# Kernel tuning notes

Measured on AMD Instinct MI355X. Metric: run time of the kernel, lower is better.

## Reference

```python
import jax, jax.numpy as jnp
import numpy as np

N_A = 50000
N_B = 50000
E = 500000
HID = 128
NEG_SLOPE = 0.2
LN_EPS = 1e-5


def _ln(x, g, b):
    mu = jnp.mean(x, axis=-1, keepdims=True)
    var = jnp.mean((x - mu) ** 2, axis=-1, keepdims=True)
    return (x - mu) * jax.lax.rsqrt(var + LN_EPS) * g + b


def _gat(x_src, x_dst, src, dst, W, a_src, a_dst, bias, H, D, n_dst):
    # PyG GATConv (shared lin for src/dst, add_self_loops=False, eval mode)
    hs = (x_src @ W).reshape(-1, H, D)              # [N_src, H, D]
    hd = (x_dst @ W).reshape(-1, H, D)              # [N_dst, H, D]
    a_s = jnp.einsum('nhd,hd->nh', hs, a_src)       # per-node src score
    a_d = jnp.einsum('nhd,hd->nh', hd, a_dst)       # per-node dst score
    e = jax.nn.leaky_relu(a_s[src] + a_d[dst], NEG_SLOPE)   # [E, H]
    m = jax.ops.segment_max(e, dst, num_segments=n_dst)     # segment softmax
    m = jnp.where(jnp.isfinite(m), m, 0.0)
    ex = jnp.exp(e - m[dst])
    s = jax.ops.segment_sum(ex, dst, num_segments=n_dst)
    alpha = ex / (s[dst] + 1e-16)                   # [E, H]
    msg = hs[src] * alpha[:, :, None]               # [E, H, D]
    out = jax.ops.segment_sum(msg, dst, num_segments=n_dst) # [N_dst, H, D]
    return out.reshape(n_dst, H * D) + bias


def setup_inputs() -> dict:
    key = jax.random.key(0)
    ks = jax.random.split(key, 32)
    f32 = jnp.float32

    def rn(k, sh, s=0.05):
        return jax.random.normal(k, sh, dtype=f32) * s

    inp = {}
    inp['x_A'] = jax.random.normal(ks[0], (N_A, 128), dtype=f32)
    inp['x_B'] = jax.random.normal(ks[1], (N_B, 64), dtype=f32)
    inp['pWA'] = rn(ks[2], (128, HID)); inp['pbA'] = rn(ks[3], (HID,))
    inp['pWB'] = rn(ks[4], (64, HID)); inp['pbB'] = rn(ks[5], (HID,))
    inp['w0ab'] = rn(ks[6], (HID, HID)); inp['as0ab'] = rn(ks[7], (4, 32))
    inp['ad0ab'] = rn(ks[8], (4, 32)); inp['b0ab'] = rn(ks[9], (HID,))
    inp['w0ba'] = rn(ks[10], (HID, HID)); inp['as0ba'] = rn(ks[11], (4, 32))
    inp['ad0ba'] = rn(ks[12], (4, 32)); inp['b0ba'] = rn(ks[13], (HID,))
    inp['w1ab'] = rn(ks[14], (HID, HID)); inp['as1ab'] = rn(ks[15], (1, HID))
    inp['ad1ab'] = rn(ks[16], (1, HID)); inp['b1ab'] = rn(ks[17], (HID,))
    inp['w1ba'] = rn(ks[18], (HID, HID)); inp['as1ba'] = rn(ks[19], (1, HID))
    inp['ad1ba'] = rn(ks[20], (1, HID)); inp['b1ba'] = rn(ks[21], (HID,))
    for i, nm in enumerate(['0A', '0B', '1A', '1B']):
        inp['g' + nm] = jnp.ones((HID,), dtype=f32)
        inp['bn' + nm] = jnp.zeros((HID,), dtype=f32)
    inp['ei_AB'] = jax.random.randint(ks[22], (2, E), 0, N_B)  # src in A, dst in B
    inp['ei_BA'] = jax.random.randint(ks[23], (2, E), 0, N_A)  # src in B, dst in A
    return inp


def reference(x_A, x_B, pWA, pbA, pWB, pbB,
              w0ab, as0ab, ad0ab, b0ab, w0ba, as0ba, ad0ba, b0ba,
              w1ab, as1ab, ad1ab, b1ab, w1ba, as1ba, ad1ba, b1ba,
              g0A, bn0A, g0B, bn0B, g1A, bn1A, g1B, bn1B,
              ei_AB, ei_BA):
    # input projections (dropout is eval-mode no-op)
    hA = x_A @ pWA + pbA
    hB = x_B @ pWB + pbB
    # layer 0: heads=4, d_head=32, concat -> 128
    pA, pB = hA, hB
    nB = _gat(hA, hB, ei_AB[0], ei_AB[1], w0ab, as0ab, ad0ab, b0ab, 4, 32, N_B)
    nA = _gat(hB, hA, ei_BA[0], ei_BA[1], w0ba, as0ba, ad0ba, b0ba, 4, 32, N_A)
    hA = jax.nn.relu(_ln(nA, g0A, bn0A)) + pA
    hB = jax.nn.relu(_ln(nB, g0B, bn0B)) + pB
    # layer 1: heads=1, out=128
    pA, pB = hA, hB
    nB = _gat(hA, hB, ei_AB[0], ei_AB[1], w1ab, as1ab, ad1ab, b1ab, 1, HID, N_B)
    nA = _gat(hB, hA, ei_BA[0], ei_BA[1], w1ba, as1ba, ad1ba, b1ba, 1, HID, N_A)
    hA = jax.nn.relu(_ln(nA, g1A, bn1A)) + pA
    hB = jax.nn.relu(_ln(nB, g1B, bn1B)) + pB
    return hA, hB
```

## Files before the change

kernel.cpp:

```cpp
#include <hip/hip_runtime.h>
#include <hip/hip_bf16.h>

using bf16 = __hip_bfloat16;
using frag8 = __attribute__((ext_vector_type(8))) short;
using f32x4 = __attribute__((ext_vector_type(4))) float;

__device__ __forceinline__ short f2bf_bits(float f) {
  bf16 h = __float2bfloat16(f);
  short s; __builtin_memcpy(&s, &h, 2); return s;
}
__device__ __forceinline__ float bfbits2f(unsigned short u) {
  unsigned uu = (unsigned)u << 16; float f; __builtin_memcpy(&f, &uu, 4); return f;
}
__device__ __forceinline__ float wred_sum(float v) {
#pragma unroll
  for (int o = 32; o; o >>= 1) v += __shfl_xor(v, o);
  return v;
}

struct ConvJob { const void* src; void* dst; int n; int mode; int ksh; };
struct ConvJobs { ConvJob j[28]; };
struct WtJob { const void* wraw; const void* adraw; bf16* out; int H; };
struct WtJobs4 { WtJob j[4]; };

__global__ __launch_bounds__(256) void prep_k(
    const unsigned* __restrict__ xdet, int* __restrict__ flag,
    ConvJobs cjobs, int ncv, WtJobs4 wjobs,
    int* __restrict__ cntA, int nA, int* __restrict__ cntB, int nB)
{
  const int b = blockIdx.x, tid = threadIdx.x;
  if (b >= ncv + 4) {
    int i = (b - (ncv + 4)) * 256 + tid;
    if (i < nA) cntA[i] = 0;
    else if (i < nA + nB) cntB[i - nA] = 0;
    return;
  }
  __shared__ int sh[256];
  int c = 0;
  for (int i = tid; i < 4096; i += 256) {
    unsigned bb = (xdet[i] >> 8) & 0x7F;
    c += (bb >= 0x3B && bb <= 0x41) ? 1 : 0;
  }
  sh[tid] = c; __syncthreads();
  for (int off = 128; off; off >>= 1) { if (tid < off) sh[tid] += sh[tid + off]; __syncthreads(); }
  const int f = (sh[0] < 2048) ? 1 : 0;
  if (b == 0 && tid == 0) flag[0] = f;

  if (b < ncv) {
    ConvJob J = cjobs.j[b];
    const int Kt = 1 << J.ksh;
    for (int i = tid; i < J.n; i += 256) {
      int si = i;
      if (J.mode == 1) { int n = i >> J.ksh, k = i & (Kt - 1); si = k * 128 + n; }
      float v = f ? ((const float*)J.src)[si] : bfbits2f(((const unsigned short*)J.src)[si]);
      if (J.mode == 1) ((bf16*)J.dst)[i] = __float2bfloat16(v);
      else             ((float*)J.dst)[i] = v;
    }
  } else {
    WtJob J = wjobs.j[b - ncv];
    const int H = J.H, D = 128 / H;
    for (int idx = tid; idx < 16 * 128; idx += 256) {
      int h = idx >> 7, k = idx & 127;
      float s = 0.f;
      if (h < H) {
        for (int d = 0; d < D; d++) {
          int n = h * D + d;
          float wv = f ? ((const float*)J.wraw)[k * 128 + n]
                       : bfbits2f(((const unsigned short*)J.wraw)[k * 128 + n]);
          float av = f ? ((const float*)J.adraw)[n]
                       : bfbits2f(((const unsigned short*)J.adraw)[n]);
          s += wv * av;
        }
      }
      J.out[idx] = __float2bfloat16(s);
    }
  }
}

__global__ void hist2_k(const int* __restrict__ dAB, const int* __restrict__ dBA, int E,
                        int* __restrict__ cntB, int* __restrict__ cntA, int geh) {
  int b = blockIdx.x;
  if (b < geh) { int i = b * 256 + threadIdx.x; if (i < E) atomicAdd(&cntB[dAB[i]], 1); }
  else { int i = (b - geh) * 256 + threadIdx.x; if (i < E) atomicAdd(&cntA[dBA[i]], 1); }
}
__device__ __forceinline__ void blocksum_body(const int* cnt, int N, int* bsum, int blk) {
  __shared__ int sh[256];
  const int tid = threadIdx.x;
  const int beg = blk * 1024;
  const int end = (beg + 1024 < N) ? beg + 1024 : N;
  int loc = 0;
  for (int i = beg + tid; i < end; i += 256) loc += cnt[i];
  sh[tid] = loc; __syncthreads();
  for (int off = 128; off; off >>= 1) { if (tid < off) sh[tid] += sh[tid + off]; __syncthreads(); }
  if (tid == 0) bsum[blk] = sh[0];
}
__global__ void blocksum2_k(const int* __restrict__ cntB, int NB, int* __restrict__ bsumB, int nbB,
                            const int* __restrict__ cntA, int NA, int* __restrict__ bsumA) {
  int b = blockIdx.x;
  if (b < nbB) blocksum_body(cntB, NB, bsumB, b);
  else         blocksum_body(cntA, NA, bsumA, b - nbB);
}
__device__ __forceinline__ void scanpart_body(int* bsum, int nb) {
  __shared__ int sh[256];
  const int tid = threadIdx.x;
  int v = (tid < nb) ? bsum[tid] : 0;
  sh[tid] = v; __syncthreads();
  for (int off = 1; off < 256; off <<= 1) {
    int x = sh[tid];
    int o = (tid >= off) ? sh[tid - off] : 0;
    __syncthreads();
    sh[tid] = x + o;
    __syncthreads();
  }
  if (tid < nb) bsum[tid] = (tid == 0) ? 0 : sh[tid - 1];
}
__global__ void scanpart2_k(int* __restrict__ bsumB, int nbB, int* __restrict__ bsumA, int nbA) {
  if (blockIdx.x == 0) scanpart_body(bsumB, nbB);
  else                 scanpart_body(bsumA, nbA);
}
__device__ __forceinline__ void writerp_body(const int* cnt, int N, const int* bsum,
                                             int* rp, int* cur, int blk) {
  __shared__ int sh[256];
  const int tid = threadIdx.x;
  const int idx0 = blk * 1024 + tid * 4;
  int c[4]; int loc = 0;
#pragma unroll
  for (int j = 0; j < 4; j++) {
    int i = idx0 + j;
    c[j] = (i < N) ? cnt[i] : 0;
    loc += c[j];
  }
  sh[tid] = loc; __syncthreads();
  for (int off = 1; off < 256; off <<= 1) {
    int x = sh[tid];
    int o = (tid >= off) ? sh[tid - off] : 0;
    __syncthreads();
    sh[tid] = x + o;
    __syncthreads();
  }
  int run = bsum[blk] + ((tid == 0) ? 0 : sh[tid - 1]);
#pragma unroll
  for (int j = 0; j < 4; j++) {
    int i = idx0 + j;
    if (i < N) { rp[i] = run; cur[i] = run; }
    run += c[j];
  }
  if (idx0 <= N - 1 && N - 1 < idx0 + 4) rp[N] = run;
}
__global__ void writerp2_k(const int* __restrict__ cntB, int NB, const int* __restrict__ bsumB,
                           int* __restrict__ rpAB, int* __restrict__ curB, int nbB,
                           const int* __restrict__ cntA, int NA, const int* __restrict__ bsumA,
                           int* __restrict__ rpBA, int* __restrict__ curA) {
  int b = blockIdx.x;
  if (b < nbB) writerp_body(cntB, NB, bsumB, rpAB, curB, b);
  else         writerp_body(cntA, NA, bsumA, rpBA, curA, b - nbB);
}
__global__ void scatter2_k(const int* __restrict__ sAB, const int* __restrict__ dAB,
                           int* __restrict__ curB, int* __restrict__ slAB,
                           const int* __restrict__ sBA, const int* __restrict__ dBA,
                           int* __restrict__ curA, int* __restrict__ slBA, int E, int geh) {
  int b = blockIdx.x;
  if (b < geh) {
    int i = b * 256 + threadIdx.x;
    if (i < E) { int d = dAB[i]; int pos = atomicAdd(&curB[d], 1); slAB[pos] = sAB[i]; }
  } else {
    int i = (b - geh) * 256 + threadIdx.x;
    if (i < E) { int d = dBA[i]; int pos = atomicAdd(&curA[d], 1); slBA[pos] = sBA[i]; }
  }
}

struct GemmJob {
  const void* Av; const bf16* WT; const float* bias; const float* avec;
  bf16* outFull; float* outScore; const int* flagp;
  const bf16* WT2; float* outScore2;
  int M, K, H, H2;
};
__global__ __launch_bounds__(256) void gemm2_k(GemmJob ja, GemmJob jb, int split) {
  const bool first = blockIdx.x < split;
  const GemmJob J = first ? ja : jb;
  const int blk = first ? blockIdx.x : blockIdx.x - split;

  __shared__ __align__(16) bf16 Wt[128 * 136];
  __shared__ __align__(16) bf16 Wt2s[16 * 136];
  const int tid = threadIdx.x;
  const int K = J.K;
  const int isf32 = J.flagp ? J.flagp[0] : 0;
  const int stride = K + 8;
  const int ksh2 = (K == 128) ? 4 : 3;
  const int kunits = K >> 3;
  for (int u = tid; u < 128 * kunits; u += 256) {
    int n = u >> ksh2, kb = u & (kunits - 1);
    frag8 v = *(const frag8*)(J.WT + n * K + kb * 8);
    *(frag8*)(Wt + n * stride + kb * 8) = v;
  }
  if (J.WT2) {
    int n = tid >> 4, kb = tid & 15;
    *(frag8*)(Wt2s + n * 136 + kb * 8) = *(const frag8*)(J.WT2 + n * 128 + kb * 8);
  }
  __syncthreads();

  const int lane = tid & 63, wave = tid >> 6;
  const int quad = lane >> 4, c = lane & 15;
  const int mbase = blk * 64 + wave * 16;
  const int arow = mbase + c;
  const bool rowOK = arow < J.M;

  f32x4 acc[8];
#pragma unroll
  for (int t = 0; t < 8; t++) acc[t] = (f32x4){0.f, 0.f, 0.f, 0.f};
  f32x4 acc2 = (f32x4){0.f, 0.f, 0.f, 0.f};

  for (int ks = 0; ks < K; ks += 32) {
    frag8 af;
    const int k0 = ks + quad * 8;
    if (rowOK) {
      if (isf32) {
        const float4* ap = (const float4*)((const float*)J.Av + (size_t)arow * K + k0);
        float4 v0 = ap[0], v1 = ap[1];
        af[0] = f2bf_bits(v0.x); af[1] = f2bf_bits(v0.y);
        af[2] = f2bf_bits(v0.z); af[3] = f2bf_bits(v0.w);
        af[4] = f2bf_bits(v1.x); af[5] = f2bf_bits(v1.y);
        af[6] = f2bf_bits(v1.z); af[7] = f2bf_bits(v1.w);
      } else {
        af = *(const frag8*)((const bf16*)J.Av + (size_t)arow * K + k0);
      }
    } else {
#pragma unroll
      for (int j = 0; j < 8; j++) af[j] = 0;
    }
#pragma unroll
    for (int t = 0; t < 8; t++) {
      frag8 bfv = *(const frag8*)(Wt + (t * 16 + c) * stride + k0);
      acc[t] = __builtin_amdgcn_mfma_f32_16x16x32_bf16(af, bfv, acc[t], 0, 0, 0);
    }
    if (J.WT2) {
      frag8 b2 = *(const frag8*)(Wt2s + c * 136 + k0);
      acc2 = __builtin_amdgcn_mfma_f32_16x16x32_bf16(af, b2, acc2, 0, 0, 0);
    }
  }

  if (J.outFull) {
#pragma unroll
    for (int t = 0; t < 8; t++) {
#pragma unroll
      for (int r = 0; r < 4; r++) {
        int orow = mbase + quad * 4 + r;
        if (orow < J.M) {
          float v = acc[t][r];
          if (J.bias) v += J.bias[t * 16 + c];
          J.outFull[(size_t)orow * 128 + t * 16 + c] = __float2bfloat16(v);
        }
      }
    }
  }
  if (J.outScore) {
    const int H = J.H;
    const int TPH = 8 / H;
    for (int hh = 0; hh < H; hh++) {
#pragma unroll
      for (int r = 0; r < 4; r++) {
        float p = 0.f;
        for (int tt = 0; tt < TPH; tt++) {
          int t = hh * TPH + tt;
          p += acc[t][r] * J.avec[t * 16 + c];
        }
#pragma unroll
        for (int off = 1; off < 16; off <<= 1) p += __shfl_xor(p, off);
        int orow = mbase + quad * 4 + r;
        if (c == 0 && orow < J.M) J.outScore[(size_t)orow * H + hh] = p;
      }
    }
  }
  if (J.outScore2) {
#pragma unroll
    for (int r = 0; r < 4; r++) {
      int orow = mbase + quad * 4 + r;
      if (c < J.H2 && orow < J.M) J.outScore2[(size_t)orow * J.H2 + c] = acc2[r];
    }
  }
}

struct AggJob {
  const int* rp; const int* srcl; const float* as_; const float* ad_;
  const bf16* hs; const float* bias; const float* gamma; const float* beta;
  const bf16* resid; bf16* outBf; void* outFinal; const int* flagp;
  int nodeBase, N;
};
template<int H, bool FINAL>
__global__ __launch_bounds__(256) void agg2_k(AggJob JA, AggJob JB, int split) {
  const bool first = blockIdx.x < split;
  const AggJob J = first ? JA : JB;
  const int blk = first ? blockIdx.x : blockIdx.x - split;

  __shared__ int   s_src[4][64];
  __shared__ float s_p[4][64 * H];
  const int wave = threadIdx.x >> 6, lane = threadIdx.x & 63;
  const int n = blk * 4 + wave;
  if (n >= J.N) return;

  const int beg = J.rp[n], end = J.rp[n + 1];
  const int myh = (H == 4) ? (lane >> 4) : 0;
  float4 adv;
  if (H == 4) adv = *(const float4*)(J.ad_ + (size_t)n * 4);
  else        adv.x = J.ad_[n];
  float sl_[H];
#pragma unroll
  for (int h = 0; h < H; h++) sl_[h] = 0.f;
  float acc0 = 0.f, acc1 = 0.f;

  for (int base = beg; base < end; base += 64) {
    const int cn = min(64, end - base);
    if (lane < cn) {
      int s = J.srcl[base + lane];
      s_src[wave][lane] = s;
      if (H == 4) {
        float4 a = *(const float4*)(J.as_ + (size_t)s * 4);
        float4 o; float v;
        v = a.x + adv.x; v = v > 0.f ? v : 0.2f * v; o.x = __expf(v);
        v = a.y + adv.y; v = v > 0.f ? v : 0.2f * v; o.y = __expf(v);
        v = a.z + adv.z; v = v > 0.f ? v : 0.2f * v; o.z = __expf(v);
        v = a.w + adv.w; v = v > 0.f ? v : 0.2f * v; o.w = __expf(v);
        *(float4*)&s_p[wave][lane * 4] = o;
        sl_[0] += o.x; sl_[1] += o.y; sl_[2] += o.z; sl_[3] += o.w;
      } else {
        float v = J.as_[s] + adv.x;
        v = v > 0.f ? v : 0.2f * v;
        float pv = __expf(v);
        s_p[wave][lane] = pv;
        sl_[0] += pv;
      }
    }
    __builtin_amdgcn_wave_barrier();
#pragma unroll 2
    for (int e = 0; e < cn; e++) {
      int src = s_src[wave][e];
      float p = s_p[wave][e * H + myh];
      unsigned u = *(const unsigned*)(J.hs + (size_t)src * 128 + 2 * lane);
      acc0 += p * bfbits2f((unsigned short)(u & 0xFFFF));
      acc1 += p * bfbits2f((unsigned short)(u >> 16));
    }
    __builtin_amdgcn_wave_barrier();
  }

  float s = 0.f;
#pragma unroll
  for (int h = 0; h < H; h++) {
    float t = wred_sum(sl_[h]);
    if (h == myh) s = t;
  }
  const float inv = 1.f / (s + 1e-16f);
  float2 bi = *(const float2*)(J.bias + 2 * lane);
  float y0 = acc0 * inv + bi.x;
  float y1 = acc1 * inv + bi.y;

  float tsum = wred_sum(y0 + y1);
  float tsq  = wred_sum(y0 * y0 + y1 * y1);
  float mu = tsum * 0.0078125f;
  float var = tsq * 0.0078125f - mu * mu;
  float rs = rsqrtf(var + 1e-5f);
  float2 ga = *(const float2*)(J.gamma + 2 * lane);
  float2 be = *(const float2*)(J.beta + 2 * lane);
  float z0 = (y0 - mu) * rs * ga.x + be.x;
  float z1 = (y1 - mu) * rs * ga.y + be.y;
  unsigned ru = *(const unsigned*)(J.resid + (size_t)n * 128 + 2 * lane);
  z0 = fmaxf(z0, 0.f) + bfbits2f((unsigned short)(ru & 0xFFFF));
  z1 = fmaxf(z1, 0.f) + bfbits2f((unsigned short)(ru >> 16));

  if constexpr (FINAL) {
    size_t oi = (size_t)(J.nodeBase + n) * 128 + 2 * lane;
    if (J.flagp[0]) {
      *(float2*)((float*)J.outFinal + oi) = make_float2(z0, z1);
    } else {
      unsigned short l0 = (unsigned short)f2bf_bits(z0);
      unsigned short l1 = (unsigned short)f2bf_bits(z1);
      *(unsigned*)((bf16*)J.outFinal + oi) = (unsigned)l0 | ((unsigned)l1 << 16);
    }
  } else {
    unsigned short l0 = (unsigned short)f2bf_bits(z0);
    unsigned short l1 = (unsigned short)f2bf_bits(z1);
    *(unsigned*)(J.outBf + (size_t)n * 128 + 2 * lane) = (unsigned)l0 | ((unsigned)l1 << 16);
  }
}

extern "C" void kernel_launch(void* const* d_in, const int* in_sizes, int n_in,
                              void* d_out, int out_size, void* d_ws, size_t ws_size,
                              hipStream_t stream)
{
  const int NA = in_sizes[0] / 128;
  const int NB = in_sizes[1] / 64;
  const int E  = in_sizes[30] / 2;
  const int* eiAB = (const int*)d_in[30];
  const int* eiBA = (const int*)d_in[31];
  const int* srcAB = eiAB;  const int* dstAB = eiAB + E;
  const int* srcBA = eiBA;  const int* dstBA = eiBA + E;

  char* w = (char*)d_ws;
  size_t used = 0;
  auto alloc = [&](size_t bytes) {
    char* p = w + used;
    used += (bytes + 255) & ~size_t(255);
    return (void*)p;
  };
  int*  flag  = (int*)alloc(256);
  bf16* WcA   = (bf16*)alloc(16384 * 2);
  bf16* WcB   = (bf16*)alloc(8192 * 2);
  bf16* Wc0ab = (bf16*)alloc(16384 * 2);
  bf16* Wc0ba = (bf16*)alloc(16384 * 2);
  bf16* Wc1ab = (bf16*)alloc(16384 * 2);
  bf16* Wc1ba = (bf16*)alloc(16384 * 2);
  bf16* Wt0ab = (bf16*)alloc(16 * 128 * 2);
  bf16* Wt0ba = (bf16*)alloc(16 * 128 * 2);
  bf16* Wt1ab = (bf16*)alloc(16 * 128 * 2);
  bf16* Wt1ba = (bf16*)alloc(16 * 128 * 2);
  float* vec  = (float*)alloc(22 * 128 * 4);
  bf16* hA    = (bf16*)alloc((size_t)NA * 128 * 2);
  bf16* hB    = (bf16*)alloc((size_t)NB * 128 * 2);
  bf16* hsAB  = (bf16*)alloc((size_t)NA * 128 * 2);
  bf16* hsBA  = (bf16*)alloc((size_t)NB * 128 * 2);
  float* asAB = (float*)alloc((size_t)NA * 4 * 4);
  float* adAB = (float*)alloc((size_t)NB * 4 * 4);
  float* asBA = (float*)alloc((size_t)NB * 4 * 4);
  float* adBA = (float*)alloc((size_t)NA * 4 * 4);
  int* rpAB = (int*)alloc((size_t)(NB + 1) * 4);
  int* slAB = (int*)alloc((size_t)E * 4);
  int* rpBA = (int*)alloc((size_t)(NA + 1) * 4);
  int* slBA = (int*)alloc((size_t)E * 4);
  int* cntA = (int*)alloc((size_t)NA * 4);
  int* curA = (int*)alloc((size_t)NA * 4);
  int* cntB = (int*)alloc((size_t)NB * 4);
  int* curB = (int*)alloc((size_t)NB * 4);
  int* bsumA = (int*)alloc(256 * 4);
  int* bsumB = (int*)alloc(256 * 4);
  if (used > ws_size) return;

  auto V = [&](int i) { return vec + 128 * i; };

  ConvJobs jobs{};
  int nj = 0;
  auto addT = [&](const void* s, void* d, int K) {
    int ksh = (K == 128) ? 7 : 6;
    jobs.j[nj++] = ConvJob{s, d, 128 * K, 1, ksh};
  };
  auto addV = [&](const void* s, void* d) { jobs.j[nj++] = ConvJob{s, d, 128, 0, 7}; };
  addT(d_in[2], WcA, 128);
  addT(d_in[4], WcB, 64);
  addT(d_in[6], Wc0ab, 128);
  addT(d_in[10], Wc0ba, 128);
  addT(d_in[14], Wc1ab, 128);
  addT(d_in[18], Wc1ba, 128);
  const int vsrc[22] = {3, 5, 7, 8, 9, 11, 12, 13, 15, 16, 17, 19, 20, 21, 22, 23, 24, 25, 26, 27, 28, 29};
  for (int i = 0; i < 22; i++) addV(d_in[vsrc[i]], V(i));

  WtJobs4 wj{};
  wj.j[0] = WtJob{d_in[6],  d_in[8],  Wt0ab, 4};
  wj.j[1] = WtJob{d_in[10], d_in[12], Wt0ba, 4};
  wj.j[2] = WtJob{d_in[14], d_in[16], Wt1ab, 1};
  wj.j[3] = WtJob{d_in[18], d_in[20], Wt1ba, 1};

  const int nz = (NA + NB + 255) / 256;
  prep_k<<<nj + 4 + nz, 256, 0, stream>>>((const unsigned*)d_in[0], flag, jobs, nj, wj,
                                          cntA, NA, cntB, NB);

  const int nbB = (NB + 1023) / 1024, nbA = (NA + 1023) / 1024;
  const int geh = (E + 255) / 256;
  hist2_k<<<2 * geh, 256, 0, stream>>>(dstAB, dstBA, E, cntB, cntA, geh);
  blocksum2_k<<<nbB + nbA, 256, 0, stream>>>(cntB, NB, bsumB, nbB, cntA, NA, bsumA);
  scanpart2_k<<<2, 256, 0, stream>>>(bsumB, nbB, bsumA, nbA);
  writerp2_k<<<nbB + nbA, 256, 0, stream>>>(cntB, NB, bsumB, rpAB, curB, nbB,
                                            cntA, NA, bsumA, rpBA, curA);
  scatter2_k<<<2 * geh, 256, 0, stream>>>(srcAB, dstAB, curB, slAB,
                                          srcBA, dstBA, curA, slBA, E, geh);

  const int gA = (NA + 63) / 64, gB = (NB + 63) / 64;
  const int aA = (NA + 3) / 4, aB = (NB + 3) / 4;

  {
    GemmJob ja{d_in[0], WcA, V(0), nullptr, hA, nullptr, flag, nullptr, nullptr, NA, 128, 1, 0};
    GemmJob jb{d_in[1], WcB, V(1), nullptr, hB, nullptr, flag, nullptr, nullptr, NB, 64, 1, 0};
    gemm2_k<<<gA + gB, 256, 0, stream>>>(ja, jb, gA);
  }
  {
    GemmJob ja{hA, Wc0ab, nullptr, V(2), hsAB, asAB, nullptr, Wt0ba, adBA, NA, 128, 4, 4};
    GemmJob jb{hB, Wc0ba, nullptr, V(5), hsBA, asBA, nullptr, Wt0ab, adAB, NB, 128, 4, 4};
    gemm2_k<<<gA + gB, 256, 0, stream>>>(ja, jb, gA);
  }
  {
    AggJob ja{rpAB, slAB, asAB, adAB, hsAB, V(4), V(16), V(17), hB, hB, nullptr, nullptr, 0, NB};
    AggJob jb{rpBA, slBA, asBA, adBA, hsBA, V(7), V(14), V(15), hA, hA, nullptr, nullptr, 0, NA};
    agg2_k<4, false><<<aB + aA, 256, 0, stream>>>(ja, jb, aB);
  }
  {
    GemmJob ja{hA, Wc1ab, nullptr, V(8),  hsAB, asAB, nullptr, Wt1ba, adBA, NA, 128, 1, 1};
    GemmJob jb{hB, Wc1ba, nullptr, V(11), hsBA, asBA, nullptr, Wt1ab, adAB, NB, 128, 1, 1};
    gemm2_k<<<gA + gB, 256, 0, stream>>>(ja, jb, gA);
  }
  {
    AggJob ja{rpAB, slAB, asAB, adAB, hsAB, V(10), V(20), V(21), hB, nullptr, d_out, flag, NA, NB};
    AggJob jb{rpBA, slBA, asBA, adBA, hsBA, V(13), V(18), V(19), hA, nullptr, d_out, flag, 0, NA};
    agg2_k<1, true><<<aB + aA, 256, 0, stream>>>(ja, jb, aB);
  }
}
```

Measured before the change: 480.5 us.

## Fuse CSR build into GEMM launches, partition scatter, split aggregation by head count

The edge histogram now runs as extra blocks inside the input-projection GEMM launch. The prefix scan is collapsed into two single-block scans that run alongside the layer-0 GEMM. This removes four separate launches and the multi-level scan. The scatter is rewritten so each block handles only one eighth of the destination range, which is meant to improve atomic and write locality. Aggregation is split into specialised 4-head and 1-head kernels that use readfirstlane scalar loads; the 1-head path drops shared-memory staging and computes the softmax inline per edge. The single-block scan is serial per thread over about 200 entries each and may become a long tail inside the GEMM launch.

```diff
diff --git a/kernel.cpp b/kernel.cpp
--- a/kernel.cpp
+++ b/kernel.cpp
@@ -16,6 +16,11 @@
 #pragma unroll
   for (int o = 32; o; o >>= 1) v += __shfl_xor(v, o);
   return v;
+}
+__device__ __forceinline__ float rfl_f(float v) {
+  int i; __builtin_memcpy(&i, &v, 4);
+  i = __builtin_amdgcn_readfirstlane(i);
+  float f; __builtin_memcpy(&f, &i, 4); return f;
 }
 
 struct ConvJob { const void* src; void* dst; int n; int mode; int ksh; };
@@ -77,109 +82,13 @@
   }
 }
 
-__global__ void hist2_k(const int* __restrict__ dAB, const int* __restrict__ dBA, int E,
-                        int* __restrict__ cntB, int* __restrict__ cntA, int geh) {
-  int b = blockIdx.x;
-  if (b < geh) { int i = b * 256 + threadIdx.x; if (i < E) atomicAdd(&cntB[dAB[i]], 1); }
-  else { int i = (b - geh) * 256 + threadIdx.x; if (i < E) atomicAdd(&cntA[dBA[i]], 1); }
-}
-__device__ __forceinline__ void blocksum_body(const int* cnt, int N, int* bsum, int blk) {
-  __shared__ int sh[256];
-  const int tid = threadIdx.x;
-  const int beg = blk * 1024;
-  const int end = (beg + 1024 < N) ? beg + 1024 : N;
-  int loc = 0;
-  for (int i = beg + tid; i < end; i += 256) loc += cnt[i];
-  sh[tid] = loc; __syncthreads();
-  for (int off = 128; off; off >>= 1) { if (tid < off) sh[tid] += sh[tid + off]; __syncthreads(); }
-  if (tid == 0) bsum[blk] = sh[0];
-}
-__global__ void blocksum2_k(const int* __restrict__ cntB, int NB, int* __restrict__ bsumB, int nbB,
-                            const int* __restrict__ cntA, int NA, int* __restrict__ bsumA) {
-  int b = blockIdx.x;
-  if (b < nbB) blocksum_body(cntB, NB, bsumB, b);
-  else         blocksum_body(cntA, NA, bsumA, b - nbB);
-}
-__device__ __forceinline__ void scanpart_body(int* bsum, int nb) {
-  __shared__ int sh[256];
-  const int tid = threadIdx.x;
-  int v = (tid < nb) ? bsum[tid] : 0;
-  sh[tid] = v; __syncthreads();
-  for (int off = 1; off < 256; off <<= 1) {
-    int x = sh[tid];
-    int o = (tid >= off) ? sh[tid - off] : 0;
-    __syncthreads();
-    sh[tid] = x + o;
-    __syncthreads();
-  }
-  if (tid < nb) bsum[tid] = (tid == 0) ? 0 : sh[tid - 1];
-}
-__global__ void scanpart2_k(int* __restrict__ bsumB, int nbB, int* __restrict__ bsumA, int nbA) {
-  if (blockIdx.x == 0) scanpart_body(bsumB, nbB);
-  else                 scanpart_body(bsumA, nbA);
-}
-__device__ __forceinline__ void writerp_body(const int* cnt, int N, const int* bsum,
-                                             int* rp, int* cur, int blk) {
-  __shared__ int sh[256];
-  const int tid = threadIdx.x;
-  const int idx0 = blk * 1024 + tid * 4;
-  int c[4]; int loc = 0;
-#pragma unroll
-  for (int j = 0; j < 4; j++) {
-    int i = idx0 + j;
-    c[j] = (i < N) ? cnt[i] : 0;
-    loc += c[j];
-  }
-  sh[tid] = loc; __syncthreads();
-  for (int off = 1; off < 256; off <<= 1) {
-    int x = sh[tid];
-    int o = (tid >= off) ? sh[tid - off] : 0;
-    __syncthreads();
-    sh[tid] = x + o;
-    __syncthreads();
-  }
-  int run = bsum[blk] + ((tid == 0) ? 0 : sh[tid - 1]);
-#pragma unroll
-  for (int j = 0; j < 4; j++) {
-    int i = idx0 + j;
-    if (i < N) { rp[i] = run; cur[i] = run; }
-    run += c[j];
-  }
-  if (idx0 <= N - 1 && N - 1 < idx0 + 4) rp[N] = run;
-}
-__global__ void writerp2_k(const int* __restrict__ cntB, int NB, const int* __restrict__ bsumB,
-                           int* __restrict__ rpAB, int* __restrict__ curB, int nbB,
-                           const int* __restrict__ cntA, int NA, const int* __restrict__ bsumA,
-                           int* __restrict__ rpBA, int* __restrict__ curA) {
-  int b = blockIdx.x;
-  if (b < nbB) writerp_body(cntB, NB, bsumB, rpAB, curB, b);
-  else         writerp_body(cntA, NA, bsumA, rpBA, curA, b - nbB);
-}
-__global__ void scatter2_k(const int* __restrict__ sAB, const int* __restrict__ dAB,
-                           int* __restrict__ curB, int* __restrict__ slAB,
-                           const int* __restrict__ sBA, const int* __restrict__ dBA,
-                           int* __restrict__ curA, int* __restrict__ slBA, int E, int geh) {
-  int b = blockIdx.x;
-  if (b < geh) {
-    int i = b * 256 + threadIdx.x;
-    if (i < E) { int d = dAB[i]; int pos = atomicAdd(&curB[d], 1); slAB[pos] = sAB[i]; }
-  } else {
-    int i = (b - geh) * 256 + threadIdx.x;
-    if (i < E) { int d = dBA[i]; int pos = atomicAdd(&curA[d], 1); slBA[pos] = sBA[i]; }
-  }
-}
-
 struct GemmJob {
   const void* Av; const bf16* WT; const float* bias; const float* avec;
   bf16* outFull; float* outScore; const int* flagp;
   const bf16* WT2; float* outScore2;
   int M, K, H, H2;
 };
-__global__ __launch_bounds__(256) void gemm2_k(GemmJob ja, GemmJob jb, int split) {
-  const bool first = blockIdx.x < split;
-  const GemmJob J = first ? ja : jb;
-  const int blk = first ? blockIdx.x : blockIdx.x - split;
-
+__device__ __forceinline__ void gemm_body(const GemmJob& J, int blk) {
   __shared__ __align__(16) bf16 Wt[128 * 136];
   __shared__ __align__(16) bf16 Wt2s[16 * 136];
   const int tid = threadIdx.x;
@@ -280,79 +189,105 @@
   }
 }
 
+__global__ __launch_bounds__(256) void histgemm_k(
+    GemmJob ja, GemmJob jb, int gsplit,
+    const int* __restrict__ dAB, const int* __restrict__ dBA, int E, int geh,
+    int* __restrict__ cntB, int* __restrict__ cntA)
+{
+  const int b = blockIdx.x;
+  if (b < 2 * geh) {
+    if (b < geh) { int i = b * 256 + threadIdx.x; if (i < E) atomicAdd(&cntB[dAB[i]], 1); }
+    else { int i = (b - geh) * 256 + threadIdx.x; if (i < E) atomicAdd(&cntA[dBA[i]], 1); }
+    return;
+  }
+  const int gb = b - 2 * geh;
+  if (gb < gsplit) gemm_body(ja, gb);
+  else             gemm_body(jb, gb - gsplit);
+}
+
+__device__ __forceinline__ void scanfull_body(const int* __restrict__ cnt, int N,
+                                              int* __restrict__ rp, int* __restrict__ cur) {
+  __shared__ int sh[256];
+  const int tid = threadIdx.x;
+  const int seg = (N + 255) / 256;
+  const int b0 = tid * seg < N ? tid * seg : N;
+  const int b1 = (tid + 1) * seg < N ? (tid + 1) * seg : N;
+  int loc = 0;
+  for (int i = b0; i < b1; i++) loc += cnt[i];
+  sh[tid] = loc; __syncthreads();
+  for (int off = 1; off < 256; off <<= 1) {
+    int x = sh[tid];
+    int o = (tid >= off) ? sh[tid - off] : 0;
+    __syncthreads();
+    sh[tid] = x + o;
+    __syncthreads();
+  }
+  int run = (tid == 0) ? 0 : sh[tid - 1];
+  for (int i = b0; i < b1; i++) { rp[i] = run; cur[i] = run; run += cnt[i]; }
+  if (tid == 255) rp[N] = run;
+}
+__global__ __launch_bounds__(256) void scangemm_k(
+    GemmJob ja, GemmJob jb, int gsplit,
+    const int* __restrict__ cntB, int NB, int* __restrict__ rpAB, int* __restrict__ curB,
+    const int* __restrict__ cntA, int NA, int* __restrict__ rpBA, int* __restrict__ curA)
+{
+  const int b = blockIdx.x;
+  if (b < 2) {
+    if (b == 0) scanfull_body(cntB, NB, rpAB, curB);
+    else        scanfull_body(cntA, NA, rpBA, curA);
+    return;
+  }
+  const int gb = b - 2;
+  if (gb < gsplit) gemm_body(ja, gb);
+  else             gemm_body(jb, gb - gsplit);
+}
+
+__global__ __launch_bounds__(256) void gemm2_k(GemmJob ja, GemmJob jb, int split) {
+  if (blockIdx.x < split) gemm_body(ja, blockIdx.x);
+  else                    gemm_body(jb, blockIdx.x - split);
+}
+
+__global__ __launch_bounds__(256) void scatter8_k(
+    const int* __restrict__ sAB, const int* __restrict__ dAB,
+    const int* __restrict__ sBA, const int* __restrict__ dBA, int E,
+    int* __restrict__ curB, int* __restrict__ slAB,
+    int* __restrict__ curA, int* __restrict__ slBA, int NB, int NA)
+{
+  const int g = blockIdx.x & 7;
+  const int sidx = blockIdx.x >> 3;
+  const int loB = (int)((long long)NB * g >> 3), hiB = (int)((long long)NB * (g + 1) >> 3);
+  const int loA = (int)((long long)NA * g >> 3), hiA = (int)((long long)NA * (g + 1) >> 3);
+  const int b0 = sidx * 2048;
+#pragma unroll
+  for (int j = 0; j < 8; j++) {
+    int i = b0 + j * 256 + threadIdx.x;
+    if (i < 2 * E) {
+      bool ab = i < E;
+      int k = ab ? i : i - E;
+      int d = ab ? dAB[k] : dBA[k];
+      int lo = ab ? loB : loA, hi = ab ? hiB : hiA;
+      if (d >= lo && d < hi) {
+        int sv = ab ? sAB[k] : sBA[k];
+        int pos = atomicAdd((ab ? curB : curA) + d, 1);
+        (ab ? slAB : slBA)[pos] = sv;
+      }
+    }
+  }
+}
+
 struct AggJob {
   const int* rp; const int* srcl; const float* as_; const float* ad_;
   const bf16* hs; const float* bias; const float* gamma; const float* beta;
   const bf16* resid; bf16* outBf; void* outFinal; const int* flagp;
   int nodeBase, N;
 };
-template<int H, bool FINAL>
-__global__ __launch_bounds__(256) void agg2_k(AggJob JA, AggJob JB, int split) {
-  const bool first = blockIdx.x < split;
-  const AggJob J = first ? JA : JB;
-  const int blk = first ? blockIdx.x : blockIdx.x - split;
-
-  __shared__ int   s_src[4][64];
-  __shared__ float s_p[4][64 * H];
-  const int wave = threadIdx.x >> 6, lane = threadIdx.x & 63;
-  const int n = blk * 4 + wave;
-  if (n >= J.N) return;
-
-  const int beg = J.rp[n], end = J.rp[n + 1];
-  const int myh = (H == 4) ? (lane >> 4) : 0;
-  float4 adv;
-  if (H == 4) adv = *(const float4*)(J.ad_ + (size_t)n * 4);
-  else        adv.x = J.ad_[n];
-  float sl_[H];
-#pragma unroll
-  for (int h = 0; h < H; h++) sl_[h] = 0.f;
-  float acc0 = 0.f, acc1 = 0.f;
-
-  for (int base = beg; base < end; base += 64) {
-    const int cn = min(64, end - base);
-    if (lane < cn) {
-      int s = J.srcl[base + lane];
-      s_src[wave][lane] = s;
-      if (H == 4) {
-        float4 a = *(const float4*)(J.as_ + (size_t)s * 4);
-        float4 o; float v;
-        v = a.x + adv.x; v = v > 0.f ? v : 0.2f * v; o.x = __expf(v);
-        v = a.y + adv.y; v = v > 0.f ? v : 0.2f * v; o.y = __expf(v);
-        v = a.z + adv.z; v = v > 0.f ? v : 0.2f * v; o.z = __expf(v);
-        v = a.w + adv.w; v = v > 0.f ? v : 0.2f * v; o.w = __expf(v);
-        *(float4*)&s_p[wave][lane * 4] = o;
-        sl_[0] += o.x; sl_[1] += o.y; sl_[2] += o.z; sl_[3] += o.w;
-      } else {
-        float v = J.as_[s] + adv.x;
-        v = v > 0.f ? v : 0.2f * v;
-        float pv = __expf(v);
-        s_p[wave][lane] = pv;
-        sl_[0] += pv;
-      }
-    }
-    __builtin_amdgcn_wave_barrier();
-#pragma unroll 2
-    for (int e = 0; e < cn; e++) {
-      int src = s_src[wave][e];
-      float p = s_p[wave][e * H + myh];
-      unsigned u = *(const unsigned*)(J.hs + (size_t)src * 128 + 2 * lane);
-      acc0 += p * bfbits2f((unsigned short)(u & 0xFFFF));
-      acc1 += p * bfbits2f((unsigned short)(u >> 16));
-    }
-    __builtin_amdgcn_wave_barrier();
-  }
-
-  float s = 0.f;
-#pragma unroll
-  for (int h = 0; h < H; h++) {
-    float t = wred_sum(sl_[h]);
-    if (h == myh) s = t;
-  }
-  const float inv = 1.f / (s + 1e-16f);
+
+template<bool FINAL>
+__device__ __forceinline__ void agg_epilogue(const AggJob& J, int n, int lane,
+                                             float inv, float acc0, float acc1) {
   float2 bi = *(const float2*)(J.bias + 2 * lane);
   float y0 = acc0 * inv + bi.x;
   float y1 = acc1 * inv + bi.y;
-
   float tsum = wred_sum(y0 + y1);
   float tsq  = wred_sum(y0 * y0 + y1 * y1);
   float mu = tsum * 0.0078125f;
@@ -365,7 +300,6 @@
   unsigned ru = *(const unsigned*)(J.resid + (size_t)n * 128 + 2 * lane);
   z0 = fmaxf(z0, 0.f) + bfbits2f((unsigned short)(ru & 0xFFFF));
   z1 = fmaxf(z1, 0.f) + bfbits2f((unsigned short)(ru >> 16));
-
   if constexpr (FINAL) {
     size_t oi = (size_t)(J.nodeBase + n) * 128 + 2 * lane;
     if (J.flagp[0]) {
@@ -380,6 +314,92 @@
     unsigned short l1 = (unsigned short)f2bf_bits(z1);
     *(unsigned*)(J.outBf + (size_t)n * 128 + 2 * lane) = (unsigned)l0 | ((unsigned)l1 << 16);
   }
+}
+
+template<bool FINAL>
+__global__ __launch_bounds__(256) void agg4_k(AggJob JA, AggJob JB, int split) {
+  const bool first = blockIdx.x < split;
+  const AggJob J = first ? JA : JB;
+  const int blk = first ? blockIdx.x : blockIdx.x - split;
+
+  __shared__ float s_p[4][64 * 4];
+  const int lane = threadIdx.x & 63;
+  const int wave = __builtin_amdgcn_readfirstlane(threadIdx.x >> 6);
+  const int n = blk * 4 + wave;
+  if (n >= J.N) return;
+
+  const int beg = __builtin_amdgcn_readfirstlane(J.rp[n]);
+  const int end = __builtin_amdgcn_readfirstlane(J.rp[n + 1]);
+  const int myh = lane >> 4;
+  const float4 adv = *(const float4*)(J.ad_ + (size_t)n * 4);
+  float sl0 = 0.f, sl1 = 0.f, sl2 = 0.f, sl3 = 0.f;
+  float acc0 = 0.f, acc1 = 0.f;
+  const int* srcp = J.srcl;
+  const bf16* hsp = J.hs;
+
+  for (int base = beg; base < end; base += 64) {
+    const int cn = (end - base < 64) ? end - base : 64;
+    if (lane < cn) {
+      int s = srcp[base + lane];
+      float4 a = *(const float4*)(J.as_ + (size_t)s * 4);
+      float4 o; float v;
+      v = a.x + adv.x; v = v > 0.f ? v : 0.2f * v; o.x = __expf(v);
+      v = a.y + adv.y; v = v > 0.f ? v : 0.2f * v; o.y = __expf(v);
+      v = a.z + adv.z; v = v > 0.f ? v : 0.2f * v; o.z = __expf(v);
+      v = a.w + adv.w; v = v > 0.f ? v : 0.2f * v; o.w = __expf(v);
+      *(float4*)&s_p[wave][lane * 4] = o;
+      sl0 += o.x; sl1 += o.y; sl2 += o.z; sl3 += o.w;
+    }
+    __builtin_amdgcn_wave_barrier();
+#pragma unroll 4
+    for (int e = 0; e < cn; e++) {
+      const int src = __builtin_amdgcn_readfirstlane(srcp[base + e]);
+      const float p = s_p[wave][e * 4 + myh];
+      const unsigned u = *(const unsigned*)(hsp + (size_t)src * 128 + 2 * lane);
+      acc0 += p * bfbits2f((unsigned short)(u & 0xFFFF));
+      acc1 += p * bfbits2f((unsigned short)(u >> 16));
+    }
+    __builtin_amdgcn_wave_barrier();
+  }
+
+  float t0 = wred_sum(sl0), t1 = wred_sum(sl1), t2 = wred_sum(sl2), t3 = wred_sum(sl3);
+  float s = (myh == 0) ? t0 : (myh == 1) ? t1 : (myh == 2) ? t2 : t3;
+  const float inv = 1.f / (s + 1e-16f);
+  agg_epilogue<FINAL>(J, n, lane, inv, acc0, acc1);
+}
+
+template<bool FINAL>
+__global__ __launch_bounds__(256) void agg1_k(AggJob JA, AggJob JB, int split) {
+  const bool first = blockIdx.x < split;
+  const AggJob J = first ? JA : JB;
+  const int blk = first ? blockIdx.x : blockIdx.x - split;
+
+  const int lane = threadIdx.x & 63;
+  const int wave = __builtin_amdgcn_readfirstlane(threadIdx.x >> 6);
+  const int n = blk * 4 + wave;
+  if (n >= J.N) return;
+
+  const int beg = __builtin_amdgcn_readfirstlane(J.rp[n]);
+  const int end = __builtin_amdgcn_readfirstlane(J.rp[n + 1]);
+  const float adn = rfl_f(J.ad_[n]);
+  float sum = 0.f, acc0 = 0.f, acc1 = 0.f;
+  const int* srcp = J.srcl;
+  const float* asp = J.as_;
+  const bf16* hsp = J.hs;
+
+#pragma unroll 4
+  for (int e = beg; e < end; e++) {
+    const int src = __builtin_amdgcn_readfirstlane(srcp[e]);
+    float v = rfl_f(asp[src]) + adn;
+    v = v > 0.f ? v : 0.2f * v;
+    const float p = __expf(v);
+    sum += p;
+    const unsigned u = *(const unsigned*)(hsp + (size_t)src * 128 + 2 * lane);
+    acc0 += p * bfbits2f((unsigned short)(u & 0xFFFF));
+    acc1 += p * bfbits2f((unsigned short)(u >> 16));
+  }
+  const float inv = 1.f / (sum + 1e-16f);
+  agg_epilogue<FINAL>(J, n, lane, inv, acc0, acc1);
 }
 
 extern "C" void kernel_launch(void* const* d_in, const int* in_sizes, int n_in,
@@ -429,8 +449,6 @@
   int* curA = (int*)alloc((size_t)NA * 4);
   int* cntB = (int*)alloc((size_t)NB * 4);
   int* curB = (int*)alloc((size_t)NB * 4);
-  int* bsumA = (int*)alloc(256 * 4);
-  int* bsumB = (int*)alloc(256 * 4);
   if (used > ws_size) return;
 
   auto V = [&](int i) { return vec + 128 * i; };
@@ -461,33 +479,32 @@
   prep_k<<<nj + 4 + nz, 256, 0, stream>>>((const unsigned*)d_in[0], flag, jobs, nj, wj,
                                           cntA, NA, cntB, NB);
 
-  const int nbB = (NB + 1023) / 1024, nbA = (NA + 1023) / 1024;
   const int geh = (E + 255) / 256;
-  hist2_k<<<2 * geh, 256, 0, stream>>>(dstAB, dstBA, E, cntB, cntA, geh);
-  blocksum2_k<<<nbB + nbA, 256, 0, stream>>>(cntB, NB, bsumB, nbB, cntA, NA, bsumA);
-  scanpart2_k<<<2, 256, 0, stream>>>(bsumB, nbB, bsumA, nbA);
-  writerp2_k<<<nbB + nbA, 256, 0, stream>>>(cntB, NB, bsumB, rpAB, curB, nbB,
-                                            cntA, NA, bsumA, rpBA, curA);
-  scatter2_k<<<2 * geh, 256, 0, stream>>>(srcAB, dstAB, curB, slAB,
-                                          srcBA, dstBA, curA, slBA, E, geh);
-
   const int gA = (NA + 63) / 64, gB = (NB + 63) / 64;
   const int aA = (NA + 3) / 4, aB = (NB + 3) / 4;
 
   {
     GemmJob ja{d_in[0], WcA, V(0), nullptr, hA, nullptr, flag, nullptr, nullptr, NA, 128, 1, 0};
     GemmJob jb{d_in[1], WcB, V(1), nullptr, hB, nullptr, flag, nullptr, nullptr, NB, 64, 1, 0};
-    gemm2_k<<<gA + gB, 256, 0, stream>>>(ja, jb, gA);
+    histgemm_k<<<2 * geh + gA + gB, 256, 0, stream>>>(ja, jb, gA, dstAB, dstBA, E, geh,
+                                                      cntB, cntA);
   }
   {
     GemmJob ja{hA, Wc0ab, nullptr, V(2), hsAB, asAB, nullptr, Wt0ba, adBA, NA, 128, 4, 4};
     GemmJob jb{hB, Wc0ba, nullptr, V(5), hsBA, asBA, nullptr, Wt0ab, adAB, NB, 128, 4, 4};
-    gemm2_k<<<gA + gB, 256, 0, stream>>>(ja, jb, gA);
+    scangemm_k<<<2 + gA + gB, 256, 0, stream>>>(ja, jb, gA,
+                                                cntB, NB, rpAB, curB,
+                                                cntA, NA, rpBA, curA);
+  }
+  {
+    const int nsl = (2 * E + 2047) / 2048;
+    scatter8_k<<<8 * nsl, 256, 0, stream>>>(srcAB, dstAB, srcBA, dstBA, E,
+                                            curB, slAB, curA, slBA, NB, NA);
   }
   {
     AggJob ja{rpAB, slAB, asAB, adAB, hsAB, V(4), V(16), V(17), hB, hB, nullptr, nullptr, 0, NB};
     AggJob jb{rpBA, slBA, asBA, adBA, hsBA, V(7), V(14), V(15), hA, hA, nullptr, nullptr, 0, NA};
-    agg2_k<4, false><<<aB + aA, 256, 0, stream>>>(ja, jb, aB);
+    agg4_k<false><<<aB + aA, 256, 0, stream>>>(ja, jb, aB);
   }
   {
     GemmJob ja{hA, Wc1ab, nullptr, V(8),  hsAB, asAB, nullptr, Wt1ba, adBA, NA, 128, 1, 1};
@@ -497,6 +514,6 @@
   {
     AggJob ja{rpAB, slAB, asAB, adAB, hsAB, V(10), V(20), V(21), hB, nullptr, d_out, flag, NA, NB};
     AggJob jb{rpBA, slBA, asBA, adBA, hsBA, V(13), V(18), V(19), hA, nullptr, d_out, flag, 0, NA};
-    agg2_k<1, true><<<aB + aA, 256, 0, stream>>>(ja, jb, aB);
-  }
-}
+    agg1_k<true><<<aB + aA, 256, 0, stream>>>(ja, jb, aB);
+  }
+}
```

Measured after the change: 591.7 us. +23.1%, slower.
